# Optimization experiments

Measured on AMD Instinct MI355X. Metric: run time of the kernel, lower is better.

The kernel has to match this reference:

```python
import jax, jax.numpy as jnp
import numpy as np

N = 50000      # nodes
E = 800000     # edges (avg degree 16)
F_IN = 64      # node_features
HID = 64       # hidden_dim
OUT = 32       # output_dim


def setup_inputs() -> dict:
    key = jax.random.key(0)
    ks = jax.random.split(key, 24)
    inp = {
        "x": jax.random.normal(ks[0], (N, F_IN), jnp.float32),
        "edge_index": jax.random.randint(ks[1], (2, E), 0, N, dtype=jnp.int64),
        "edge_weight": jax.random.uniform(ks[2], (E,), jnp.float32),
    }
    def w(k, i, o):
        return jax.random.normal(k, (i, o), jnp.float32) * 0.05
    ki = 3
    # 6 ChebConv (K=2) weight pairs + bias: gates z, r, h for x-path and h-path
    for nm in ["xz", "hz", "xr", "hr", "xh", "hh"]:
        din = F_IN if nm[0] == "x" else HID
        inp[f"W{nm}0"] = w(ks[ki], din, HID); ki += 1
        inp[f"W{nm}1"] = w(ks[ki], din, HID); ki += 1
        inp[f"b{nm}"] = jnp.zeros((HID,), jnp.float32)
    inp["Wlin"] = w(ks[ki], HID, OUT); ki += 1
    inp["blin"] = jnp.zeros((OUT,), jnp.float32)
    return inp


def reference(x, edge_index, edge_weight,
              Wxz0, Wxz1, bxz, Whz0, Whz1, bhz,
              Wxr0, Wxr1, bxr, Whr0, Whr1, bhr,
              Wxh0, Wxh1, bxh, Whh0, Whh1, bhh,
              Wlin, blin):
    src, dst = edge_index[0], edge_index[1]
    # scaled Chebyshev Laplacian (lambda_max=2, sym norm): L_hat = -D^{-1/2} A D^{-1/2}, diag 0
    deg = jax.ops.segment_sum(edge_weight, src, num_segments=N)
    deg_safe = jnp.where(deg > 0, deg, 1.0)
    dinv = jnp.where(deg > 0, jax.lax.rsqrt(deg_safe), 0.0)
    norm = -dinv[src] * edge_weight * dinv[dst]  # [E]

    def prop(v):  # L_hat @ v via gather-scatter
        return jax.ops.segment_sum(norm[:, None] * v[src], dst, num_segments=N)

    def cheb(v, W0, W1, b):  # ChebConv K=2: T0(v) W0 + T1(v) W1 + b
        return v @ W0 + prop(v) @ W1 + b

    H = jnp.zeros((N, HID), x.dtype)  # GConvGRU initial state
    Z = jax.nn.sigmoid(cheb(x, Wxz0, Wxz1, bxz) + cheb(H, Whz0, Whz1, bhz))
    R = jax.nn.sigmoid(cheb(x, Wxr0, Wxr1, bxr) + cheb(H, Whr0, Whr1, bhr))
    Ht = jnp.tanh(cheb(x, Wxh0, Wxh1, bxh) + cheb(H * R, Whh0, Whh1, bhh))
    H = Z * H + (1.0 - Z) * Ht

    h = H @ Wlin + blin
    # F.normalize(p=2, dim=1)
    return h / jnp.maximum(jnp.linalg.norm(h, axis=1, keepdims=True), 1e-12)
```

## Files before the change

### kernel.cpp

```cpp
#include <hip/hip_runtime.h>
#include <math.h>

#define N_NODES 50000
#define F 64
#define OUTF 32
#define NX4 (N_NODES * 16)
#define NPREP (16384 + 2048 + 128 + 32)
#define NCURZ 12500
#define CAP 64

#define HCHUNK 64
#define HR 25000

typedef __bf16 v8bf __attribute__((ext_vector_type(8)));
typedef float v4f __attribute__((ext_vector_type(4)));

static __device__ __forceinline__ unsigned short f2bf(float f) {
    union { float f; unsigned u; } v; v.f = f;
    unsigned r = v.u + 0x7FFFu + ((v.u >> 16) & 1u);
    return (unsigned short)(r >> 16);
}
static __device__ __forceinline__ float bf2f(unsigned short h) {
    union { unsigned u; float f; } v; v.u = ((unsigned)h) << 16;
    return v.f;
}

__global__ void pre_kernel(const float4* __restrict__ x4, uint2* __restrict__ xb4,
                           uint4* __restrict__ cur4,
                           const float* __restrict__ Wxz0, const float* __restrict__ Wxz1,
                           const float* __restrict__ Wxh0, const float* __restrict__ Wxh1,
                           const float* __restrict__ Wlin,
                           const float* __restrict__ bxz, const float* __restrict__ bhz,
                           const float* __restrict__ bxh, const float* __restrict__ bhh,
                           const float* __restrict__ blin,
                           unsigned short* __restrict__ Bt, unsigned short* __restrict__ Wlt,
                           float* __restrict__ bzc, float* __restrict__ blc) {
    int i = blockIdx.x * 256 + threadIdx.x;
    if (i < NX4) {
        float4 v = x4[i];
        uint2 o;
        o.x = (unsigned)f2bf(v.x) | ((unsigned)f2bf(v.y) << 16);
        o.y = (unsigned)f2bf(v.z) | ((unsigned)f2bf(v.w) << 16);
        xb4[i] = o;
    } else if (i < NX4 + NCURZ) {
        cur4[i - NX4] = make_uint4(0u, 0u, 0u, 0u);
    } else {
        int idx = i - NX4 - NCURZ;
        if (idx < 16384) {
            int k = idx & 127, n = idx >> 7;
            float v;
            if (k < 64) v = (n < 64) ? Wxz0[k * 64 + n] : Wxh0[k * 64 + (n - 64)];
            else        v = (n < 64) ? Wxz1[(k - 64) * 64 + n] : Wxh1[(k - 64) * 64 + (n - 64)];
            Bt[n * 128 + k] = f2bf(v);
        } else if (idx < 16384 + 2048) {
            int j = idx - 16384; int k = j & 63, n = j >> 6;
            Wlt[n * 64 + k] = f2bf(Wlin[k * 32 + n]);
        } else if (idx < 16384 + 2048 + 128) {
            int j = idx - 16384 - 2048;
            bzc[j] = (j < 64) ? (bxz[j] + bhz[j]) : (bxh[j - 64] + bhh[j - 64]);
        } else if (idx < NPREP) {
            int j = idx - 16384 - 2048 - 128;
            blc[j] = blin[j];
        }
    }
}

__launch_bounds__(1024)
__global__ void histw_kernel(const int* __restrict__ src, const float* __restrict__ ew,
                             float* __restrict__ partW, int E) {
    __shared__ float sdeg[HR];
    int b = blockIdx.x, tid = threadIdx.x;
    int chunk = b >> 1, half = b & 1;
    int nbase = half * HR;
    int epb = (E + HCHUNK - 1) / HCHUNK;
    int lo = chunk * epb, hi = min(lo + epb, E);
    for (int i = tid; i < HR; i += 1024) sdeg[i] = 0.f;
    __syncthreads();
    for (int e = lo + tid; e < hi; e += 1024) {
        int s = src[e];
        unsigned ls = (unsigned)(s - nbase);
        if (ls < HR) atomicAdd(&sdeg[ls], ew[e]);
    }
    __syncthreads();
    for (int i = tid; i < HR; i += 1024)
        partW[(size_t)chunk * N_NODES + nbase + i] = sdeg[i];
}

__global__ void reducew_kernel(const float* __restrict__ partW, float* __restrict__ dinv) {
    int i = blockIdx.x * 256 + threadIdx.x;
    if (i >= N_NODES) return;
    float s = 0.f;
    #pragma unroll
    for (int b = 0; b < HCHUNK; ++b) s += partW[(size_t)b * N_NODES + i];
    dinv[i] = s > 0.f ? rsqrtf(s) : 0.f;
}

__global__ void place_kernel(const int* __restrict__ src, const int* __restrict__ dst,
                             const float* __restrict__ w, const float* __restrict__ dinv,
                             unsigned* __restrict__ cursor, unsigned* __restrict__ rec, int E) {
    int e = blockIdx.x * 256 + threadIdx.x;
    if (e >= E) return;
    int s = src[e], d = dst[e];
    if ((unsigned)s >= N_NODES || (unsigned)d >= N_NODES) return;
    float coef = -dinv[s] * w[e] * dinv[d];
    unsigned pos = atomicAdd(&cursor[d], 1u);
    if (pos < CAP)
        rec[((size_t)d << 6) + pos] = (unsigned)s | ((unsigned)f2bf(coef) << 16);
}

__launch_bounds__(256)
__global__ void accum_kernel(const unsigned* __restrict__ rec, const unsigned* __restrict__ cursor,
                             const unsigned short* __restrict__ xb, unsigned short* __restrict__ Pb) {
    int n = blockIdx.x * 4 + (threadIdx.x >> 6);
    int lane = threadIdx.x & 63;
    int cnt = min((int)cursor[n], CAP);
    unsigned r = (lane < cnt) ? rec[((size_t)n << 6) + lane] : 0u;
    float acc = 0.f;
    for (int j = 0; j < cnt; j += 8) {
        unsigned rv[8]; float xv[8];
        #pragma unroll
        for (int t = 0; t < 8; ++t) rv[t] = __shfl(r, j + t);
        #pragma unroll
        for (int t = 0; t < 8; ++t) xv[t] = bf2f(xb[(size_t)(rv[t] & 0xFFFFu) * 64 + lane]);
        #pragma unroll
        for (int t = 0; t < 8; ++t) acc = fmaf(bf2f((unsigned short)(rv[t] >> 16)), xv[t], acc);
    }
    Pb[(size_t)n * 64 + lane] = f2bf(acc);
}

__launch_bounds__(256, 2)
__global__ void dense_kernel(const unsigned short* __restrict__ xb, const unsigned short* __restrict__ Pb,
                             const unsigned short* __restrict__ Bt, const unsigned short* __restrict__ Wlt,
                             const float* __restrict__ bzc, const float* __restrict__ blc,
                             float* __restrict__ out) {
    __shared__ unsigned short Bs[128 * 136];
    __shared__ unsigned short Wls[32 * 80];
    __shared__ unsigned short Hs[4][16 * 80];
    __shared__ float bzs[128], bls[32];

    int tid = threadIdx.x;
    for (int c = tid; c < 4096; c += 256) {
        int n = c >> 5; int k4 = (c & 31) * 4;
        *(uint2*)&Bs[n * 136 + k4] = *(const uint2*)&Bt[n * 128 + k4];
    }
    for (int c = tid; c < 512; c += 256) {
        int n = c >> 4; int k4 = (c & 15) * 4;
        *(uint2*)&Wls[n * 80 + k4] = *(const uint2*)&Wlt[n * 64 + k4];
    }
    if (tid < 128) bzs[tid] = bzc[tid];
    if (tid < 32) bls[tid] = blc[tid];
    __syncthreads();

    int wv = tid >> 6, lane = tid & 63;
    int nl = lane & 15, q = lane >> 4;
    int ngroups = (N_NODES + 63) / 64;

    for (int g = blockIdx.x; g < ngroups; g += gridDim.x) {
        int rowbase = g * 64 + wv * 16;
        int arow = rowbase + nl; if (arow >= N_NODES) arow = N_NODES - 1;

        v4f acc[8];
        #pragma unroll
        for (int i = 0; i < 8; ++i) acc[i] = (v4f)(0.f);

        #pragma unroll
        for (int kk = 0; kk < 4; ++kk) {
            int k0 = kk * 32 + q * 8;
            const unsigned short* ap = (kk < 2) ? (xb + (size_t)arow * 64 + k0)
                                                : (Pb + (size_t)arow * 64 + (k0 - 64));
            v8bf a = *(const v8bf*)ap;
            #pragma unroll
            for (int tn = 0; tn < 8; ++tn) {
                v8bf b = *(const v8bf*)&Bs[(tn * 16 + nl) * 136 + kk * 32 + q * 8];
                acc[tn] = __builtin_amdgcn_mfma_f32_16x16x32_bf16(a, b, acc[tn], 0, 0, 0);
            }
        }

        #pragma unroll
        for (int tn = 0; tn < 4; ++tn) {
            int n = tn * 16 + nl;
            float bz = bzs[n], bh = bzs[64 + n];
            #pragma unroll
            for (int r = 0; r < 4; ++r) {
                float z = acc[tn][r] + bz;
                float h = acc[tn + 4][r] + bh;
                float sg = 1.f / (1.f + __expf(-z));
                float th = 1.f - 2.f / (__expf(2.f * h) + 1.f);
                int m = q * 4 + r;
                Hs[wv][m * 80 + n] = f2bf((1.f - sg) * th);
            }
        }

        v4f acc2[2];
        acc2[0] = (v4f)(0.f); acc2[1] = (v4f)(0.f);
        #pragma unroll
        for (int kk = 0; kk < 2; ++kk) {
            v8bf a = *(const v8bf*)&Hs[wv][nl * 80 + kk * 32 + q * 8];
            #pragma unroll
            for (int tn = 0; tn < 2; ++tn) {
                v8bf b = *(const v8bf*)&Wls[(tn * 16 + nl) * 80 + kk * 32 + q * 8];
                acc2[tn] = __builtin_amdgcn_mfma_f32_16x16x32_bf16(a, b, acc2[tn], 0, 0, 0);
            }
        }

        float o0[4], o1[4];
        #pragma unroll
        for (int r = 0; r < 4; ++r) {
            o0[r] = acc2[0][r] + bls[nl];
            o1[r] = acc2[1][r] + bls[16 + nl];
        }
        #pragma unroll
        for (int r = 0; r < 4; ++r) {
            float ss = o0[r] * o0[r] + o1[r] * o1[r];
            ss += __shfl_xor(ss, 1);
            ss += __shfl_xor(ss, 2);
            ss += __shfl_xor(ss, 4);
            ss += __shfl_xor(ss, 8);
            float dn = fmaxf(sqrtf(ss), 1e-12f);
            int node = rowbase + q * 4 + r;
            if (node < N_NODES) {
                out[node * 32 + nl] = o0[r] / dn;
                out[node * 32 + 16 + nl] = o1[r] / dn;
            }
        }
    }
}

extern "C" void kernel_launch(void* const* d_in, const int* in_sizes, int n_in,
                              void* d_out, int out_size, void* d_ws, size_t ws_size,
                              hipStream_t stream) {
    const float* x    = (const float*)d_in[0];
    const int*   ei   = (const int*)d_in[1];
    const float* ew   = (const float*)d_in[2];
    const float* Wxz0 = (const float*)d_in[3];
    const float* Wxz1 = (const float*)d_in[4];
    const float* bxz  = (const float*)d_in[5];
    const float* bhz  = (const float*)d_in[8];
    const float* Wxh0 = (const float*)d_in[15];
    const float* Wxh1 = (const float*)d_in[16];
    const float* bxh  = (const float*)d_in[17];
    const float* bhh  = (const float*)d_in[20];
    const float* Wlin = (const float*)d_in[21];
    const float* blin = (const float*)d_in[22];
    float* out = (float*)d_out;

    int E = in_sizes[2];
    const int* src = ei;
    const int* dst = ei + E;

    char* base = (char*)d_ws;
    float*          dinv   = (float*)(base + 0);
    unsigned short* xb     = (unsigned short*)(base + 200000);
    unsigned short* Pb     = (unsigned short*)(base + 6600000);
    float*          partW  = (float*)(base + 13000000);
    unsigned*       rec    = (unsigned*)(base + 13000000);
    char* p = base + 25800000;
    unsigned short* Bt     = (unsigned short*)p;      p += 128 * 128 * 2;
    unsigned short* Wlt    = (unsigned short*)p;      p += 32 * 64 * 2;
    float*          bzc    = (float*)p;               p += 128 * 4;
    float*          blc    = (float*)p;
    unsigned*       cursor = (unsigned*)(base + 25840000);

    pre_kernel<<<(NX4 + NCURZ + NPREP + 255) / 256, 256, 0, stream>>>(
        (const float4*)x, (uint2*)xb, (uint4*)cursor,
        Wxz0, Wxz1, Wxh0, Wxh1, Wlin, bxz, bhz, bxh, bhh, blin,
        Bt, Wlt, bzc, blc);

    histw_kernel<<<HCHUNK * 2, 1024, 0, stream>>>(src, ew, partW, E);
    reducew_kernel<<<(N_NODES + 255) / 256, 256, 0, stream>>>(partW, dinv);

    place_kernel<<<(E + 255) / 256, 256, 0, stream>>>(src, dst, ew, dinv, cursor, rec, E);

    accum_kernel<<<N_NODES / 4, 256, 0, stream>>>(rec, cursor, xb, Pb);

    dense_kernel<<<512, 256, 0, stream>>>(xb, Pb, Bt, Wlt, bzc, blc, out);
}
```

Baseline: 222.9 us.

## Replace global-atomic edge placement with per-chunk dst histogram and LDS cursors

Adds a destination-count histogram, computed per edge chunk and node range inside the degree-histogram launch. The reduce kernel then turns these counts into per-chunk exclusive offsets and total in-degree cursors. The place kernel uses those offsets with shared-memory atomics instead of global atomics on cursor[d], and the separate cursor zeroing in pre_kernel goes away. The intent is to cut global atomic contention and traffic. In exchange, each place block scans its whole edge chunk and keeps only 1/8 of the edges, so src/dst reads are repeated eight times, and the per-chunk offset arrays add extra memory traffic.

```diff
diff --git a/kernel.cpp b/kernel.cpp
--- a/kernel.cpp
+++ b/kernel.cpp
@@ -6,11 +6,14 @@
 #define OUTF 32
 #define NX4 (N_NODES * 16)
 #define NPREP (16384 + 2048 + 128 + 32)
-#define NCURZ 12500
 #define CAP 64
 
 #define HCHUNK 64
 #define HR 25000
+
+#define HC2 32
+#define SPL 8
+#define HR2 6250
 
 typedef __bf16 v8bf __attribute__((ext_vector_type(8)));
 typedef float v4f __attribute__((ext_vector_type(4)));
@@ -26,7 +29,6 @@
 }
 
 __global__ void pre_kernel(const float4* __restrict__ x4, uint2* __restrict__ xb4,
-                           uint4* __restrict__ cur4,
                            const float* __restrict__ Wxz0, const float* __restrict__ Wxz1,
                            const float* __restrict__ Wxh0, const float* __restrict__ Wxh1,
                            const float* __restrict__ Wlin,
@@ -42,10 +44,8 @@
         o.x = (unsigned)f2bf(v.x) | ((unsigned)f2bf(v.y) << 16);
         o.y = (unsigned)f2bf(v.z) | ((unsigned)f2bf(v.w) << 16);
         xb4[i] = o;
-    } else if (i < NX4 + NCURZ) {
-        cur4[i - NX4] = make_uint4(0u, 0u, 0u, 0u);
     } else {
-        int idx = i - NX4 - NCURZ;
+        int idx = i - NX4;
         if (idx < 16384) {
             int k = idx & 127, n = idx >> 7;
             float v;
@@ -66,46 +66,87 @@
 }
 
 __launch_bounds__(1024)
-__global__ void histw_kernel(const int* __restrict__ src, const float* __restrict__ ew,
-                             float* __restrict__ partW, int E) {
+__global__ void hist_kernel(const int* __restrict__ src, const float* __restrict__ ew,
+                            const int* __restrict__ dst,
+                            float* __restrict__ partW, unsigned* __restrict__ partC, int E) {
     __shared__ float sdeg[HR];
     int b = blockIdx.x, tid = threadIdx.x;
-    int chunk = b >> 1, half = b & 1;
-    int nbase = half * HR;
-    int epb = (E + HCHUNK - 1) / HCHUNK;
-    int lo = chunk * epb, hi = min(lo + epb, E);
-    for (int i = tid; i < HR; i += 1024) sdeg[i] = 0.f;
-    __syncthreads();
-    for (int e = lo + tid; e < hi; e += 1024) {
-        int s = src[e];
-        unsigned ls = (unsigned)(s - nbase);
-        if (ls < HR) atomicAdd(&sdeg[ls], ew[e]);
-    }
-    __syncthreads();
-    for (int i = tid; i < HR; i += 1024)
-        partW[(size_t)chunk * N_NODES + nbase + i] = sdeg[i];
-}
-
-__global__ void reducew_kernel(const float* __restrict__ partW, float* __restrict__ dinv) {
+    if (b < 128) {
+        int chunk = b >> 1, half = b & 1;
+        int nbase = half * HR;
+        int epb = (E + HCHUNK - 1) / HCHUNK;
+        int lo = chunk * epb, hi = min(lo + epb, E);
+        for (int i = tid; i < HR; i += 1024) sdeg[i] = 0.f;
+        __syncthreads();
+        for (int e = lo + tid; e < hi; e += 1024) {
+            int s = src[e];
+            unsigned ls = (unsigned)(s - nbase);
+            if (ls < HR) atomicAdd(&sdeg[ls], ew[e]);
+        }
+        __syncthreads();
+        for (int i = tid; i < HR; i += 1024)
+            partW[(size_t)chunk * N_NODES + nbase + i] = sdeg[i];
+    } else {
+        unsigned* cnt = (unsigned*)sdeg;
+        int b2 = b - 128;
+        int chunk = b2 >> 3, split = b2 & 7;
+        int nbase = split * HR2;
+        int epb = (E + HC2 - 1) / HC2;
+        int lo = chunk * epb, hi = min(lo + epb, E);
+        for (int i = tid; i < HR2; i += 1024) cnt[i] = 0u;
+        __syncthreads();
+        for (int e = lo + tid; e < hi; e += 1024) {
+            unsigned ls = (unsigned)(dst[e] - nbase);
+            if (ls < HR2) atomicAdd(&cnt[ls], 1u);
+        }
+        __syncthreads();
+        for (int i = tid; i < HR2; i += 1024)
+            partC[(size_t)chunk * N_NODES + nbase + i] = cnt[i];
+    }
+}
+
+__global__ void reducew_kernel(const float* __restrict__ partW, unsigned* __restrict__ partC,
+                               float* __restrict__ dinv, unsigned* __restrict__ cursor) {
     int i = blockIdx.x * 256 + threadIdx.x;
     if (i >= N_NODES) return;
     float s = 0.f;
     #pragma unroll
     for (int b = 0; b < HCHUNK; ++b) s += partW[(size_t)b * N_NODES + i];
     dinv[i] = s > 0.f ? rsqrtf(s) : 0.f;
-}
-
+    unsigned run = 0u;
+    #pragma unroll
+    for (int c = 0; c < HC2; ++c) {
+        unsigned v = partC[(size_t)c * N_NODES + i];
+        partC[(size_t)c * N_NODES + i] = run;
+        run += v;
+    }
+    cursor[i] = run;
+}
+
+__launch_bounds__(1024)
 __global__ void place_kernel(const int* __restrict__ src, const int* __restrict__ dst,
                              const float* __restrict__ w, const float* __restrict__ dinv,
-                             unsigned* __restrict__ cursor, unsigned* __restrict__ rec, int E) {
-    int e = blockIdx.x * 256 + threadIdx.x;
-    if (e >= E) return;
-    int s = src[e], d = dst[e];
-    if ((unsigned)s >= N_NODES || (unsigned)d >= N_NODES) return;
-    float coef = -dinv[s] * w[e] * dinv[d];
-    unsigned pos = atomicAdd(&cursor[d], 1u);
-    if (pos < CAP)
-        rec[((size_t)d << 6) + pos] = (unsigned)s | ((unsigned)f2bf(coef) << 16);
+                             const unsigned* __restrict__ offs, unsigned* __restrict__ rec, int E) {
+    __shared__ unsigned curs[HR2];
+    int b = blockIdx.x, tid = threadIdx.x;
+    int chunk = b >> 3, split = b & 7;
+    int nbase = split * HR2;
+    for (int i = tid; i < HR2; i += 1024)
+        curs[i] = offs[(size_t)chunk * N_NODES + nbase + i];
+    __syncthreads();
+    int epb = (E + HC2 - 1) / HC2;
+    int lo = chunk * epb, hi = min(lo + epb, E);
+    for (int e = lo + tid; e < hi; e += 1024) {
+        int d = dst[e];
+        unsigned ls = (unsigned)(d - nbase);
+        if (ls < HR2) {
+            int s = src[e];
+            float coef = -dinv[s] * w[e] * dinv[d];
+            unsigned pos = atomicAdd(&curs[ls], 1u);
+            if (pos < CAP)
+                rec[((size_t)d << 6) + pos] = (unsigned)s | ((unsigned)f2bf(coef) << 16);
+        }
+    }
 }
 
 __launch_bounds__(256)
@@ -251,6 +292,7 @@
     char* base = (char*)d_ws;
     float*          dinv   = (float*)(base + 0);
     unsigned short* xb     = (unsigned short*)(base + 200000);
+    unsigned*       partC  = (unsigned*)(base + 6600000);
     unsigned short* Pb     = (unsigned short*)(base + 6600000);
     float*          partW  = (float*)(base + 13000000);
     unsigned*       rec    = (unsigned*)(base + 13000000);
@@ -261,15 +303,16 @@
     float*          blc    = (float*)p;
     unsigned*       cursor = (unsigned*)(base + 25840000);
 
-    pre_kernel<<<(NX4 + NCURZ + NPREP + 255) / 256, 256, 0, stream>>>(
-        (const float4*)x, (uint2*)xb, (uint4*)cursor,
+    pre_kernel<<<(NX4 + NPREP + 255) / 256, 256, 0, stream>>>(
+        (const float4*)x, (uint2*)xb,
         Wxz0, Wxz1, Wxh0, Wxh1, Wlin, bxz, bhz, bxh, bhh, blin,
         Bt, Wlt, bzc, blc);
 
-    histw_kernel<<<HCHUNK * 2, 1024, 0, stream>>>(src, ew, partW, E);
-    reducew_kernel<<<(N_NODES + 255) / 256, 256, 0, stream>>>(partW, dinv);
-
-    place_kernel<<<(E + 255) / 256, 256, 0, stream>>>(src, dst, ew, dinv, cursor, rec, E);
+    hist_kernel<<<128 + HC2 * SPL, 1024, 0, stream>>>(src, ew, dst, partW, partC, E);
+
+    reducew_kernel<<<(N_NODES + 255) / 256, 256, 0, stream>>>(partW, partC, dinv, cursor);
+
+    place_kernel<<<HC2 * SPL, 1024, 0, stream>>>(src, dst, ew, dinv, partC, rec, E);
 
     accum_kernel<<<N_NODES / 4, 256, 0, stream>>>(rec, cursor, xb, Pb);
 
```

Result: faster. 200.0 us (-10.3%).

## Merge preprocessing, degree, and edge placement into one cooperative kernel

Applied to the files above, without the earlier changes.

Replaces four separate launches (conversion/prep, weighted degree histogram, reduction, edge placement) with one cooperative kernel that uses grid syncs between phases. Edge placement now uses per-chunk destination counts and prefix offsets held in shared memory, so slot atomics go to LDS instead of a global cursor array. This removes launch overhead and global atomic contention. In exchange it adds a second histogram pass over dst, grid-wide barriers, and a fixed grid of 256 blocks of 1024 threads, which limits parallelism in the streaming phases.

```diff
diff --git a/kernel.cpp b/kernel.cpp
--- a/kernel.cpp
+++ b/kernel.cpp
@@ -1,16 +1,19 @@
 #include <hip/hip_runtime.h>
+#include <hip/hip_cooperative_groups.h>
 #include <math.h>
+
+namespace cg = cooperative_groups;
 
 #define N_NODES 50000
 #define F 64
 #define OUTF 32
 #define NX4 (N_NODES * 16)
 #define NPREP (16384 + 2048 + 128 + 32)
-#define NCURZ 12500
 #define CAP 64
 
-#define HCHUNK 64
-#define HR 25000
+#define CH 64
+#define QS 4
+#define QR 12500
 
 typedef __bf16 v8bf __attribute__((ext_vector_type(8)));
 typedef float v4f __attribute__((ext_vector_type(4)));
@@ -25,87 +28,115 @@
     return v.f;
 }
 
-__global__ void pre_kernel(const float4* __restrict__ x4, uint2* __restrict__ xb4,
-                           uint4* __restrict__ cur4,
-                           const float* __restrict__ Wxz0, const float* __restrict__ Wxz1,
-                           const float* __restrict__ Wxh0, const float* __restrict__ Wxh1,
-                           const float* __restrict__ Wlin,
-                           const float* __restrict__ bxz, const float* __restrict__ bhz,
-                           const float* __restrict__ bxh, const float* __restrict__ bhh,
-                           const float* __restrict__ blin,
-                           unsigned short* __restrict__ Bt, unsigned short* __restrict__ Wlt,
-                           float* __restrict__ bzc, float* __restrict__ blc) {
-    int i = blockIdx.x * 256 + threadIdx.x;
-    if (i < NX4) {
-        float4 v = x4[i];
-        uint2 o;
-        o.x = (unsigned)f2bf(v.x) | ((unsigned)f2bf(v.y) << 16);
-        o.y = (unsigned)f2bf(v.z) | ((unsigned)f2bf(v.w) << 16);
-        xb4[i] = o;
-    } else if (i < NX4 + NCURZ) {
-        cur4[i - NX4] = make_uint4(0u, 0u, 0u, 0u);
-    } else {
-        int idx = i - NX4 - NCURZ;
-        if (idx < 16384) {
-            int k = idx & 127, n = idx >> 7;
-            float v;
-            if (k < 64) v = (n < 64) ? Wxz0[k * 64 + n] : Wxh0[k * 64 + (n - 64)];
-            else        v = (n < 64) ? Wxz1[(k - 64) * 64 + n] : Wxh1[(k - 64) * 64 + (n - 64)];
-            Bt[n * 128 + k] = f2bf(v);
-        } else if (idx < 16384 + 2048) {
-            int j = idx - 16384; int k = j & 63, n = j >> 6;
-            Wlt[n * 64 + k] = f2bf(Wlin[k * 32 + n]);
-        } else if (idx < 16384 + 2048 + 128) {
-            int j = idx - 16384 - 2048;
-            bzc[j] = (j < 64) ? (bxz[j] + bhz[j]) : (bxh[j - 64] + bhh[j - 64]);
-        } else if (idx < NPREP) {
-            int j = idx - 16384 - 2048 - 128;
-            blc[j] = blin[j];
-        }
-    }
-}
-
 __launch_bounds__(1024)
-__global__ void histw_kernel(const int* __restrict__ src, const float* __restrict__ ew,
-                             float* __restrict__ partW, int E) {
-    __shared__ float sdeg[HR];
-    int b = blockIdx.x, tid = threadIdx.x;
-    int chunk = b >> 1, half = b & 1;
-    int nbase = half * HR;
-    int epb = (E + HCHUNK - 1) / HCHUNK;
+__global__ void coop_kernel(const float4* __restrict__ x4, uint2* __restrict__ xb4,
+                            const int* __restrict__ src, const int* __restrict__ dst,
+                            const float* __restrict__ ew,
+                            const float* __restrict__ Wxz0, const float* __restrict__ Wxz1,
+                            const float* __restrict__ Wxh0, const float* __restrict__ Wxh1,
+                            const float* __restrict__ Wlin,
+                            const float* __restrict__ bxz, const float* __restrict__ bhz,
+                            const float* __restrict__ bxh, const float* __restrict__ bhh,
+                            const float* __restrict__ blin,
+                            unsigned short* __restrict__ Bt, unsigned short* __restrict__ Wlt,
+                            float* __restrict__ bzc, float* __restrict__ blc,
+                            float* __restrict__ partW, unsigned short* __restrict__ partC,
+                            float* __restrict__ dinv, unsigned* __restrict__ cursor,
+                            unsigned* __restrict__ rec, int E) {
+    __shared__ float smf[QR];
+    unsigned* smu = (unsigned*)smf;
+
+    int tid = threadIdx.x, b = blockIdx.x;
+    int gt = b * 1024 + tid;
+
+    for (int i = gt; i < NX4 + NPREP; i += 256 * 1024) {
+        if (i < NX4) {
+            float4 v = x4[i];
+            uint2 o;
+            o.x = (unsigned)f2bf(v.x) | ((unsigned)f2bf(v.y) << 16);
+            o.y = (unsigned)f2bf(v.z) | ((unsigned)f2bf(v.w) << 16);
+            xb4[i] = o;
+        } else {
+            int idx = i - NX4;
+            if (idx < 16384) {
+                int k = idx & 127, n = idx >> 7;
+                float v;
+                if (k < 64) v = (n < 64) ? Wxz0[k * 64 + n] : Wxh0[k * 64 + (n - 64)];
+                else        v = (n < 64) ? Wxz1[(k - 64) * 64 + n] : Wxh1[(k - 64) * 64 + (n - 64)];
+                Bt[n * 128 + k] = f2bf(v);
+            } else if (idx < 16384 + 2048) {
+                int j = idx - 16384; int k = j & 63, n = j >> 6;
+                Wlt[n * 64 + k] = f2bf(Wlin[k * 32 + n]);
+            } else if (idx < 16384 + 2048 + 128) {
+                int j = idx - 16384 - 2048;
+                bzc[j] = (j < 64) ? (bxz[j] + bhz[j]) : (bxh[j - 64] + bhh[j - 64]);
+            } else if (idx < NPREP) {
+                int j = idx - 16384 - 2048 - 128;
+                blc[j] = blin[j];
+            }
+        }
+    }
+
+    int chunk = b >> 2, qs = b & 3;
+    int nbase = qs * QR;
+    int epb = (E + CH - 1) / CH;
     int lo = chunk * epb, hi = min(lo + epb, E);
-    for (int i = tid; i < HR; i += 1024) sdeg[i] = 0.f;
+
+    for (int i = tid; i < QR; i += 1024) smf[i] = 0.f;
     __syncthreads();
     for (int e = lo + tid; e < hi; e += 1024) {
         int s = src[e];
         unsigned ls = (unsigned)(s - nbase);
-        if (ls < HR) atomicAdd(&sdeg[ls], ew[e]);
-    }
-    __syncthreads();
-    for (int i = tid; i < HR; i += 1024)
-        partW[(size_t)chunk * N_NODES + nbase + i] = sdeg[i];
-}
-
-__global__ void reducew_kernel(const float* __restrict__ partW, float* __restrict__ dinv) {
-    int i = blockIdx.x * 256 + threadIdx.x;
-    if (i >= N_NODES) return;
-    float s = 0.f;
-    #pragma unroll
-    for (int b = 0; b < HCHUNK; ++b) s += partW[(size_t)b * N_NODES + i];
-    dinv[i] = s > 0.f ? rsqrtf(s) : 0.f;
-}
-
-__global__ void place_kernel(const int* __restrict__ src, const int* __restrict__ dst,
-                             const float* __restrict__ w, const float* __restrict__ dinv,
-                             unsigned* __restrict__ cursor, unsigned* __restrict__ rec, int E) {
-    int e = blockIdx.x * 256 + threadIdx.x;
-    if (e >= E) return;
-    int s = src[e], d = dst[e];
-    if ((unsigned)s >= N_NODES || (unsigned)d >= N_NODES) return;
-    float coef = -dinv[s] * w[e] * dinv[d];
-    unsigned pos = atomicAdd(&cursor[d], 1u);
-    if (pos < CAP)
-        rec[((size_t)d << 6) + pos] = (unsigned)s | ((unsigned)f2bf(coef) << 16);
+        if (ls < QR) atomicAdd(&smf[ls], ew[e]);
+    }
+    __syncthreads();
+    for (int i = tid; i < QR; i += 1024)
+        partW[(size_t)chunk * N_NODES + nbase + i] = smf[i];
+    __syncthreads();
+
+    for (int i = tid; i < QR; i += 1024) smu[i] = 0u;
+    __syncthreads();
+    for (int e = lo + tid; e < hi; e += 1024) {
+        unsigned ls = (unsigned)(dst[e] - nbase);
+        if (ls < QR) atomicAdd(&smu[ls], 1u);
+    }
+    __syncthreads();
+    for (int i = tid; i < QR; i += 1024)
+        partC[(size_t)chunk * N_NODES + nbase + i] = (unsigned short)smu[i];
+
+    cg::this_grid().sync();
+
+    if (gt < N_NODES) {
+        float s = 0.f;
+        #pragma unroll
+        for (int c = 0; c < CH; ++c) s += partW[(size_t)c * N_NODES + gt];
+        dinv[gt] = s > 0.f ? rsqrtf(s) : 0.f;
+        unsigned run = 0u;
+        #pragma unroll
+        for (int c = 0; c < CH; ++c) {
+            unsigned v = partC[(size_t)c * N_NODES + gt];
+            partC[(size_t)c * N_NODES + gt] = (unsigned short)run;
+            run += v;
+        }
+        cursor[gt] = run;
+    }
+
+    cg::this_grid().sync();
+
+    for (int i = tid; i < QR; i += 1024)
+        smu[i] = (unsigned)partC[(size_t)chunk * N_NODES + nbase + i];
+    __syncthreads();
+    for (int e = lo + tid; e < hi; e += 1024) {
+        int d = dst[e];
+        unsigned ls = (unsigned)(d - nbase);
+        if (ls < QR) {
+            int s = src[e];
+            float coef = -dinv[s] * ew[e] * dinv[d];
+            unsigned pos = atomicAdd(&smu[ls], 1u);
+            if (pos < CAP)
+                rec[((size_t)d << 6) + pos] = (unsigned)s | ((unsigned)f2bf(coef) << 16);
+        }
+    }
 }
 
 __launch_bounds__(256)
@@ -253,23 +284,28 @@
     unsigned short* xb     = (unsigned short*)(base + 200000);
     unsigned short* Pb     = (unsigned short*)(base + 6600000);
     float*          partW  = (float*)(base + 13000000);
-    unsigned*       rec    = (unsigned*)(base + 13000000);
-    char* p = base + 25800000;
+    unsigned short* partC  = (unsigned short*)(base + 25800000);
+    unsigned*       rec    = (unsigned*)(base + 32200000);
+    char* p = base + 45000000;
     unsigned short* Bt     = (unsigned short*)p;      p += 128 * 128 * 2;
     unsigned short* Wlt    = (unsigned short*)p;      p += 32 * 64 * 2;
     float*          bzc    = (float*)p;               p += 128 * 4;
     float*          blc    = (float*)p;
-    unsigned*       cursor = (unsigned*)(base + 25840000);
-
-    pre_kernel<<<(NX4 + NCURZ + NPREP + 255) / 256, 256, 0, stream>>>(
-        (const float4*)x, (uint2*)xb, (uint4*)cursor,
-        Wxz0, Wxz1, Wxh0, Wxh1, Wlin, bxz, bhz, bxh, bhh, blin,
-        Bt, Wlt, bzc, blc);
-
-    histw_kernel<<<HCHUNK * 2, 1024, 0, stream>>>(src, ew, partW, E);
-    reducew_kernel<<<(N_NODES + 255) / 256, 256, 0, stream>>>(partW, dinv);
-
-    place_kernel<<<(E + 255) / 256, 256, 0, stream>>>(src, dst, ew, dinv, cursor, rec, E);
+    unsigned*       cursor = (unsigned*)(base + 45100000);
+
+    const float4* x4 = (const float4*)x;
+    uint2*        xb4 = (uint2*)xb;
+
+    void* kargs[] = {
+        (void*)&x4, (void*)&xb4, (void*)&src, (void*)&dst, (void*)&ew,
+        (void*)&Wxz0, (void*)&Wxz1, (void*)&Wxh0, (void*)&Wxh1, (void*)&Wlin,
+        (void*)&bxz, (void*)&bhz, (void*)&bxh, (void*)&bhh, (void*)&blin,
+        (void*)&Bt, (void*)&Wlt, (void*)&bzc, (void*)&blc,
+        (void*)&partW, (void*)&partC, (void*)&dinv, (void*)&cursor,
+        (void*)&rec, (void*)&E
+    };
+    hipLaunchCooperativeKernel((const void*)coop_kernel, dim3(256), dim3(1024),
+                               kargs, 0, stream);
 
     accum_kernel<<<N_NODES / 4, 256, 0, stream>>>(rec, cursor, xb, Pb);
 
```

Result: slower. 297.5 us (+33.5%).

## Fuse prep with packed degree/count histograms and use per-chunk shared-memory cursors for placement

Applied to the files above, without the earlier changes.

Merges the bf16 conversion/weight prep with the degree histogram into one kernel. The histogram now packs fixed-point 16-bit weighted degrees and 8-bit in-degree counts into shared memory, so one block covers all nodes. A reduce kernel computes dinv and an exclusive prefix of per-chunk counts. Placement then runs per edge chunk with shared-memory atomics instead of global atomics on a cursor array. This removes global atomic contention and one launch, but it quantizes edge weights to 1/512 and caps per-node counts at 255, both of which can overflow or lose accuracy.

```diff
diff --git a/kernel.cpp b/kernel.cpp
--- a/kernel.cpp
+++ b/kernel.cpp
@@ -6,11 +6,12 @@
 #define OUTF 32
 #define NX4 (N_NODES * 16)
 #define NPREP (16384 + 2048 + 128 + 32)
-#define NCURZ 12500
 #define CAP 64
 
-#define HCHUNK 64
-#define HR 25000
+#define CH 128
+#define NW2 25000
+#define NC4 12500
+#define PREGRID 256
 
 typedef __bf16 v8bf __attribute__((ext_vector_type(8)));
 typedef float v4f __attribute__((ext_vector_type(4)));
@@ -25,95 +26,131 @@
     return v.f;
 }
 
-__global__ void pre_kernel(const float4* __restrict__ x4, uint2* __restrict__ xb4,
-                           uint4* __restrict__ cur4,
-                           const float* __restrict__ Wxz0, const float* __restrict__ Wxz1,
-                           const float* __restrict__ Wxh0, const float* __restrict__ Wxh1,
-                           const float* __restrict__ Wlin,
-                           const float* __restrict__ bxz, const float* __restrict__ bhz,
-                           const float* __restrict__ bxh, const float* __restrict__ bhh,
-                           const float* __restrict__ blin,
-                           unsigned short* __restrict__ Bt, unsigned short* __restrict__ Wlt,
-                           float* __restrict__ bzc, float* __restrict__ blc) {
-    int i = blockIdx.x * 256 + threadIdx.x;
-    if (i < NX4) {
-        float4 v = x4[i];
-        uint2 o;
-        o.x = (unsigned)f2bf(v.x) | ((unsigned)f2bf(v.y) << 16);
-        o.y = (unsigned)f2bf(v.z) | ((unsigned)f2bf(v.w) << 16);
-        xb4[i] = o;
-    } else if (i < NX4 + NCURZ) {
-        cur4[i - NX4] = make_uint4(0u, 0u, 0u, 0u);
-    } else {
-        int idx = i - NX4 - NCURZ;
-        if (idx < 16384) {
-            int k = idx & 127, n = idx >> 7;
-            float v;
-            if (k < 64) v = (n < 64) ? Wxz0[k * 64 + n] : Wxh0[k * 64 + (n - 64)];
-            else        v = (n < 64) ? Wxz1[(k - 64) * 64 + n] : Wxh1[(k - 64) * 64 + (n - 64)];
-            Bt[n * 128 + k] = f2bf(v);
-        } else if (idx < 16384 + 2048) {
-            int j = idx - 16384; int k = j & 63, n = j >> 6;
-            Wlt[n * 64 + k] = f2bf(Wlin[k * 32 + n]);
-        } else if (idx < 16384 + 2048 + 128) {
-            int j = idx - 16384 - 2048;
-            bzc[j] = (j < 64) ? (bxz[j] + bhz[j]) : (bxh[j - 64] + bhh[j - 64]);
-        } else if (idx < NPREP) {
-            int j = idx - 16384 - 2048 - 128;
-            blc[j] = blin[j];
-        }
-    }
-}
-
 __launch_bounds__(1024)
-__global__ void histw_kernel(const int* __restrict__ src, const float* __restrict__ ew,
-                             float* __restrict__ partW, int E) {
-    __shared__ float sdeg[HR];
-    int b = blockIdx.x, tid = threadIdx.x;
-    int chunk = b >> 1, half = b & 1;
-    int nbase = half * HR;
-    int epb = (E + HCHUNK - 1) / HCHUNK;
-    int lo = chunk * epb, hi = min(lo + epb, E);
-    for (int i = tid; i < HR; i += 1024) sdeg[i] = 0.f;
+__global__ void prehist_kernel(const float4* __restrict__ x4, uint2* __restrict__ xb4,
+                               const int* __restrict__ src, const int* __restrict__ dst,
+                               const float* __restrict__ ew,
+                               const float* __restrict__ Wxz0, const float* __restrict__ Wxz1,
+                               const float* __restrict__ Wxh0, const float* __restrict__ Wxh1,
+                               const float* __restrict__ Wlin,
+                               const float* __restrict__ bxz, const float* __restrict__ bhz,
+                               const float* __restrict__ bxh, const float* __restrict__ bhh,
+                               const float* __restrict__ blin,
+                               unsigned short* __restrict__ Bt, unsigned short* __restrict__ Wlt,
+                               float* __restrict__ bzc, float* __restrict__ blc,
+                               unsigned* __restrict__ partW32, unsigned* __restrict__ partC32,
+                               int E) {
+    __shared__ unsigned sm[NW2 + NC4];
+    int tid = threadIdx.x, b = blockIdx.x;
+
+    for (int i = b * 1024 + tid; i < NX4 + NPREP; i += PREGRID * 1024) {
+        if (i < NX4) {
+            float4 v = x4[i];
+            uint2 o;
+            o.x = (unsigned)f2bf(v.x) | ((unsigned)f2bf(v.y) << 16);
+            o.y = (unsigned)f2bf(v.z) | ((unsigned)f2bf(v.w) << 16);
+            xb4[i] = o;
+        } else {
+            int idx = i - NX4;
+            if (idx < 16384) {
+                int k = idx & 127, n = idx >> 7;
+                float v;
+                if (k < 64) v = (n < 64) ? Wxz0[k * 64 + n] : Wxh0[k * 64 + (n - 64)];
+                else        v = (n < 64) ? Wxz1[(k - 64) * 64 + n] : Wxh1[(k - 64) * 64 + (n - 64)];
+                Bt[n * 128 + k] = f2bf(v);
+            } else if (idx < 16384 + 2048) {
+                int j = idx - 16384; int k = j & 63, n = j >> 6;
+                Wlt[n * 64 + k] = f2bf(Wlin[k * 32 + n]);
+            } else if (idx < 16384 + 2048 + 128) {
+                int j = idx - 16384 - 2048;
+                bzc[j] = (j < 64) ? (bxz[j] + bhz[j]) : (bxh[j - 64] + bhh[j - 64]);
+            } else if (idx < NPREP) {
+                int j = idx - 16384 - 2048 - 128;
+                blc[j] = blin[j];
+            }
+        }
+    }
+
+    if (b >= CH) return;
+
+    int epb = (E + CH - 1) / CH;
+    int lo = b * epb, hi = min(lo + epb, E);
+    for (int i = tid; i < NW2 + NC4; i += 1024) sm[i] = 0u;
     __syncthreads();
     for (int e = lo + tid; e < hi; e += 1024) {
-        int s = src[e];
-        unsigned ls = (unsigned)(s - nbase);
-        if (ls < HR) atomicAdd(&sdeg[ls], ew[e]);
+        unsigned s = (unsigned)src[e], d = (unsigned)dst[e];
+        float w = ew[e];
+        unsigned wv = (unsigned)(w * 512.f + 0.5f);
+        atomicAdd(&sm[s >> 1], wv << ((s & 1u) << 4));
+        atomicAdd(&sm[NW2 + (d >> 2)], 1u << ((d & 3u) << 3));
     }
     __syncthreads();
-    for (int i = tid; i < HR; i += 1024)
-        partW[(size_t)chunk * N_NODES + nbase + i] = sdeg[i];
-}
-
-__global__ void reducew_kernel(const float* __restrict__ partW, float* __restrict__ dinv) {
-    int i = blockIdx.x * 256 + threadIdx.x;
-    if (i >= N_NODES) return;
-    float s = 0.f;
-    #pragma unroll
-    for (int b = 0; b < HCHUNK; ++b) s += partW[(size_t)b * N_NODES + i];
-    dinv[i] = s > 0.f ? rsqrtf(s) : 0.f;
-}
-
+    unsigned* pw = partW32 + (size_t)b * NW2;
+    for (int i = tid; i < NW2; i += 1024) pw[i] = sm[i];
+    unsigned* pc = partC32 + (size_t)b * NC4;
+    for (int i = tid; i < NC4; i += 1024) pc[i] = sm[NW2 + i];
+}
+
+__global__ void reducew_kernel(const unsigned* __restrict__ partW32, unsigned* __restrict__ partC32,
+                               float* __restrict__ dinv, unsigned* __restrict__ cursor32) {
+    int j = blockIdx.x * 256 + threadIdx.x;
+    if (j >= NC4) return;
+    unsigned d0 = 0u, d1 = 0u, d2 = 0u, d3 = 0u;
+    #pragma unroll 8
+    for (int c = 0; c < CH; ++c) {
+        unsigned w0 = partW32[(size_t)c * NW2 + 2 * j];
+        unsigned w1 = partW32[(size_t)c * NW2 + 2 * j + 1];
+        d0 += w0 & 0xFFFFu; d1 += w0 >> 16;
+        d2 += w1 & 0xFFFFu; d3 += w1 >> 16;
+    }
+    float4 dv;
+    dv.x = d0 ? rsqrtf((float)d0 * 0.001953125f) : 0.f;
+    dv.y = d1 ? rsqrtf((float)d1 * 0.001953125f) : 0.f;
+    dv.z = d2 ? rsqrtf((float)d2 * 0.001953125f) : 0.f;
+    dv.w = d3 ? rsqrtf((float)d3 * 0.001953125f) : 0.f;
+    *(float4*)(dinv + 4 * j) = dv;
+
+    unsigned r0 = 0u, r1 = 0u, r2 = 0u, r3 = 0u;
+    #pragma unroll 8
+    for (int c = 0; c < CH; ++c) {
+        unsigned cw = partC32[(size_t)c * NC4 + j];
+        partC32[(size_t)c * NC4 + j] = (r0 & 0xFFu) | ((r1 & 0xFFu) << 8)
+                                     | ((r2 & 0xFFu) << 16) | ((r3 & 0xFFu) << 24);
+        r0 += cw & 0xFFu; r1 += (cw >> 8) & 0xFFu;
+        r2 += (cw >> 16) & 0xFFu; r3 += (cw >> 24) & 0xFFu;
+    }
+    cursor32[j] = min(r0, 255u) | (min(r1, 255u) << 8)
+                | (min(r2, 255u) << 16) | (min(r3, 255u) << 24);
+}
+
+__launch_bounds__(1024)
 __global__ void place_kernel(const int* __restrict__ src, const int* __restrict__ dst,
                              const float* __restrict__ w, const float* __restrict__ dinv,
-                             unsigned* __restrict__ cursor, unsigned* __restrict__ rec, int E) {
-    int e = blockIdx.x * 256 + threadIdx.x;
-    if (e >= E) return;
-    int s = src[e], d = dst[e];
-    if ((unsigned)s >= N_NODES || (unsigned)d >= N_NODES) return;
-    float coef = -dinv[s] * w[e] * dinv[d];
-    unsigned pos = atomicAdd(&cursor[d], 1u);
-    if (pos < CAP)
-        rec[((size_t)d << 6) + pos] = (unsigned)s | ((unsigned)f2bf(coef) << 16);
+                             const unsigned* __restrict__ offs32, unsigned* __restrict__ rec, int E) {
+    __shared__ unsigned curs[NC4];
+    int b = blockIdx.x, tid = threadIdx.x;
+    const unsigned* o = offs32 + (size_t)b * NC4;
+    for (int i = tid; i < NC4; i += 1024) curs[i] = o[i];
+    __syncthreads();
+    int epb = (E + CH - 1) / CH;
+    int lo = b * epb, hi = min(lo + epb, E);
+    for (int e = lo + tid; e < hi; e += 1024) {
+        unsigned s = (unsigned)src[e], d = (unsigned)dst[e];
+        float coef = -dinv[s] * w[e] * dinv[d];
+        unsigned sh = (d & 3u) << 3;
+        unsigned old = atomicAdd(&curs[d >> 2], 1u << sh);
+        unsigned pos = (old >> sh) & 0xFFu;
+        if (pos < CAP)
+            rec[((size_t)d << 6) + pos] = s | ((unsigned)f2bf(coef) << 16);
+    }
 }
 
 __launch_bounds__(256)
-__global__ void accum_kernel(const unsigned* __restrict__ rec, const unsigned* __restrict__ cursor,
+__global__ void accum_kernel(const unsigned* __restrict__ rec, const unsigned char* __restrict__ cursor8,
                              const unsigned short* __restrict__ xb, unsigned short* __restrict__ Pb) {
     int n = blockIdx.x * 4 + (threadIdx.x >> 6);
     int lane = threadIdx.x & 63;
-    int cnt = min((int)cursor[n], CAP);
+    int cnt = min((int)cursor8[n], CAP);
     unsigned r = (lane < cnt) ? rec[((size_t)n << 6) + lane] : 0u;
     float acc = 0.f;
     for (int j = 0; j < cnt; j += 8) {
@@ -252,26 +289,26 @@
     float*          dinv   = (float*)(base + 0);
     unsigned short* xb     = (unsigned short*)(base + 200000);
     unsigned short* Pb     = (unsigned short*)(base + 6600000);
-    float*          partW  = (float*)(base + 13000000);
-    unsigned*       rec    = (unsigned*)(base + 13000000);
-    char* p = base + 25800000;
+    unsigned*       partW32= (unsigned*)(base + 13000000);
+    unsigned*       partC32= (unsigned*)(base + 25800000);
+    unsigned*       rec    = (unsigned*)(base + 32200000);
+    char* p = base + 45000000;
     unsigned short* Bt     = (unsigned short*)p;      p += 128 * 128 * 2;
     unsigned short* Wlt    = (unsigned short*)p;      p += 32 * 64 * 2;
     float*          bzc    = (float*)p;               p += 128 * 4;
     float*          blc    = (float*)p;
-    unsigned*       cursor = (unsigned*)(base + 25840000);
-
-    pre_kernel<<<(NX4 + NCURZ + NPREP + 255) / 256, 256, 0, stream>>>(
-        (const float4*)x, (uint2*)xb, (uint4*)cursor,
+    unsigned*       cursor32 = (unsigned*)(base + 45100000);
+
+    prehist_kernel<<<PREGRID, 1024, 0, stream>>>(
+        (const float4*)x, (uint2*)xb, src, dst, ew,
         Wxz0, Wxz1, Wxh0, Wxh1, Wlin, bxz, bhz, bxh, bhh, blin,
-        Bt, Wlt, bzc, blc);
-
-    histw_kernel<<<HCHUNK * 2, 1024, 0, stream>>>(src, ew, partW, E);
-    reducew_kernel<<<(N_NODES + 255) / 256, 256, 0, stream>>>(partW, dinv);
-
-    place_kernel<<<(E + 255) / 256, 256, 0, stream>>>(src, dst, ew, dinv, cursor, rec, E);
-
-    accum_kernel<<<N_NODES / 4, 256, 0, stream>>>(rec, cursor, xb, Pb);
+        Bt, Wlt, bzc, blc, partW32, partC32, E);
+
+    reducew_kernel<<<(NC4 + 255) / 256, 256, 0, stream>>>(partW32, partC32, dinv, cursor32);
+
+    place_kernel<<<CH, 1024, 0, stream>>>(src, dst, ew, dinv, partC32, rec, E);
+
+    accum_kernel<<<N_NODES / 4, 256, 0, stream>>>(rec, (const unsigned char*)cursor32, xb, Pb);
 
     dense_kernel<<<512, 256, 0, stream>>>(xb, Pb, Bt, Wlt, bzc, blc, out);
 }
```

After: 192.7 us. 13.5% less time.
